# Kernel tuning notes

Hardware: AMD Instinct MI355X
Metric: run time of the kernel (lower is better)

The kernel has to match this reference:

```python
import jax, jax.numpy as jnp
import numpy as np
from jax.scipy.linalg import solve_triangular

N, K, D = 131072, 8, 32  # samples, clusters, dims


def setup_inputs() -> dict:
    key = jax.random.key(0)
    k1, k2, k3, k4 = jax.random.split(key, 4)
    return {
        "X": jax.random.normal(k1, (N, D), dtype=jnp.float32),
        "mu": jax.random.normal(k2, (K, D), dtype=jnp.float32),
        "L": jax.random.normal(k3, (K, D, D), dtype=jnp.float32),
        "weights": jax.random.normal(k4, (K,), dtype=jnp.float32),
        "it": 0,
    }


def _mixture_log_likelihoods(X, mu, L, weights):
    K_, D_ = mu.shape
    LOG2PI = float(np.log(2.0 * np.pi))
    # update_covariances: A_k = L_k L_k^T + I  (always SPD -> cholesky succeeds)
    A = jnp.einsum('kab,kcb->kac', L, L) + jnp.eye(D_, dtype=L.dtype)
    Lc = jnp.linalg.cholesky(A)            # [K,D,D] lower Cholesky factors
    invLc = jnp.linalg.inv(Lc)             # [K,D,D]
    # all cluster pairs (cartesian_prod order: i outer, j inner)
    ii, jj = [g.reshape(-1) for g in jnp.meshgrid(jnp.arange(K_), jnp.arange(K_), indexing='ij')]
    Si, Sj = Lc[ii], Lc[jj]                # NOTE: original uses the CHOLESKY FACTORS here
    invSi, invSj = invLc[ii], invLc[jj]
    mui, muj = mu[ii], mu[jj]
    # _gaussian_product: sigma = inv(inv(Si)+inv(Sj)); mu = sigma @ (inv(Si) mu_i + inv(Sj) mu_j)
    sigma = jnp.linalg.inv(invSi + invSj)                      # [P,D,D]
    rhs = jnp.einsum('pab,pb->pa', invSi, mui) + jnp.einsum('pab,pb->pa', invSj, muj)
    mu_p = jnp.einsum('pab,pb->pa', sigma, rhs)                # [P,D]
    # _product_z: log(1/sqrt(det(2*pi*(Si+Sj))) * exp(-0.5 dmu^T inv(Si+Sj) dmu))
    S = Si + Sj
    dmu = mui - muj
    quad = -0.5 * jnp.einsum('pa,pab,pb->p', dmu, jnp.linalg.inv(S), dmu)
    z = -0.5 * jnp.log(jnp.linalg.det(2.0 * np.pi * S)) + quad  # [P]
    # _unormalised_pdf: lower-triangular solve against sigma (only lower triangle used)
    diff = X[None, :, :] - mu_p[:, None, :]                    # [P,N,D]
    m = solve_triangular(sigma, jnp.swapaxes(diff, 1, 2), lower=True)  # [P,D,N]
    ll = -0.5 * (jnp.sum(m * m, axis=1) + D_ * LOG2PI
                 + jnp.log(jnp.linalg.det(sigma))[:, None])    # [P,N]
    logw = jax.nn.log_softmax(weights)                         # softmax weights, then log
    logprob = z[:, None] + ll + logw[ii][:, None] + logw[jj][:, None]  # [P,N]
    return jnp.log(jnp.sum(jnp.exp(logprob), axis=0))          # [N]


def reference(X, mu, L, weights, it):
    ll = _mixture_log_likelihoods(X, mu, L, weights)
    return jax.scipy.special.logsumexp(ll, axis=0)  # scalar
```

## Files before the change

kernel.cpp:

```cpp
#include <hip/hip_runtime.h>

#define D 32
#define K 8
#define NPAIR 36
#define PROWS 576

#define PMOFF 0
#define WOFF 4608
#define C2OFF 4864
#define CMAXOFF 4900
#define LCOFF 4928
#define PARTOFF 13120

typedef float v2f __attribute__((ext_vector_type(2)));

__host__ __device__ constexpr int gidx(int i, int j) {
    return i * 8 + j - i * (i + 1) / 2;
}
__host__ __device__ constexpr int proff(int r) {
    return 4 * (r / 4 + 1) * (2 * (r / 4) + (r % 4));
}

__global__ __launch_bounds__(64) void setup1_kernel(
    const float* __restrict__ mu, const float* __restrict__ L,
    float* __restrict__ ws)
{
    __shared__ float sA[D][D + 1];
    __shared__ float sLc[D][D + 1];
    __shared__ float sI[D][D + 1];
    const int k = blockIdx.x;
    const int tid = threadIdx.x;
    const int i = tid & 31;

    for (int e = tid; e < D * D; e += 64) sI[e >> 5][e & 31] = L[k * D * D + e];
    __syncthreads();

    for (int e = tid; e < D * D; e += 64) {
        const int a = e >> 5, c = e & 31;
        float s = (a == c) ? 1.0f : 0.0f;
        #pragma unroll
        for (int b = 0; b < D; ++b) s = fmaf(sI[a][b], sI[c][b], s);
        sA[a][c] = s;
    }
    __syncthreads();

    float lrow[D];
    #pragma unroll
    for (int j = 0; j < D; ++j) {
        if (i == j) {
            float s = sA[j][j];
            #pragma unroll
            for (int b = 0; b < j; ++b) s = fmaf(-lrow[b], lrow[b], s);
            const float d = sqrtf(s);
            lrow[j] = d;
            #pragma unroll
            for (int b = 0; b < j; ++b) sLc[j][b] = lrow[b];
            sLc[j][j] = d;
        }
        __syncthreads();
        if (i > j) {
            float s = sA[i][j];
            #pragma unroll
            for (int b = 0; b < j; ++b) s = fmaf(-lrow[b], sLc[j][b], s);
            lrow[j] = s / sLc[j][j];
        }
    }
    __syncthreads();

    for (int e = tid; e < D * D; e += 64) {
        const int r = e >> 5, c = e & 31;
        ws[LCOFF + k * D * D + e] = (c <= r) ? sLc[r][c] : 0.0f;
    }

    {
        const int j = i;
        #pragma unroll
        for (int ii = 0; ii < D; ++ii) {
            float s = (ii == j) ? 1.0f : 0.0f;
            #pragma unroll
            for (int b = 0; b < ii; ++b) s = fmaf(-sLc[ii][b], sI[b][j], s);
            const float cii = s / sLc[ii][ii];
            sI[ii][j] = cii;
            const int w4 = 4 * (ii / 4 + 1);
            if (j < w4) ws[PMOFF + k * PROWS + proff(ii) + j] = cii;
        }
    }
    __syncthreads();

    {
        float s = 0.0f;
        #pragma unroll
        for (int b = 0; b < D; ++b) s = fmaf(sI[i][b], mu[k * D + b], s);
        ws[WOFF + k * D + i] = s;
    }
}

#define SLC(kk, r, c) sLc2[(kk) * 1024 + (r) * 32 + (c)]

__global__ __launch_bounds__(64) void setup2_kernel(
    const float* __restrict__ mu, const float* __restrict__ weights,
    float* __restrict__ ws)
{
    __shared__ float sLc2[K * D * D];
    __shared__ float sLogw[K];
    __shared__ float sCp[NPAIR];
    __shared__ float sCmax;
    const int tid = threadIdx.x;

    {
        const float4* src = (const float4*)(ws + LCOFF);
        float4* dst = (float4*)sLc2;
        for (int e = tid; e < K * D * D / 4; e += 64) dst[e] = src[e];
    }
    if (tid == 0) {
        float m = -INFINITY;
        for (int t = 0; t < K; ++t) m = fmaxf(m, weights[t]);
        float s = 0.0f;
        for (int t = 0; t < K; ++t) s += expf(weights[t] - m);
        const float lse = m + logf(s);
        for (int t = 0; t < K; ++t) sLogw[t] = weights[t] - lse;
    }
    __syncthreads();

    if (tid < NPAIR) {
        int tt = tid, pi = 0;
        while (tt >= (K - pi)) { tt -= (K - pi); ++pi; }
        const int pj = pi + tt;
        const float LOG2PI = 1.8378770664093453f;
        float sumlogS = 0.0f, logdetsig = 0.0f;
        #pragma unroll
        for (int r = 0; r < D; ++r) {
            const float di = SLC(pi, r, r), dj = SLC(pj, r, r);
            sumlogS += logf(di + dj);
            logdetsig -= logf(1.0f / di + 1.0f / dj);
        }
        float v[D];
        float quad_acc = 0.0f;
        #pragma unroll
        for (int r = 0; r < D; ++r) {
            const float d0 = mu[pi * D + r] - mu[pj * D + r];
            float s = d0;
            #pragma unroll
            for (int b = 0; b < r; ++b)
                s = fmaf(-(SLC(pi, r, b) + SLC(pj, r, b)), v[b], s);
            v[r] = s / (SLC(pi, r, r) + SLC(pj, r, r));
            quad_acc = fmaf(d0, v[r], quad_acc);
        }
        const float quad = -0.5f * quad_acc;
        float c = quad - 0.5f * sumlogS - (float)D * LOG2PI - 0.5f * logdetsig
                  + sLogw[pi] + sLogw[pj];
        if (pi < pj) c += 0.6931471805599453f;
        sCp[tid] = c;
    }
    __syncthreads();
    if (tid == 0) {
        float m = -INFINITY;
        for (int t = 0; t < NPAIR; ++t) m = fmaxf(m, sCp[t]);
        sCmax = m;
        ws[CMAXOFF] = m;
    }
    __syncthreads();
    if (tid < NPAIR)
        ws[C2OFF + tid] = (sCp[tid] - sCmax) * 1.4426950408889634f;
}

__global__ __launch_bounds__(256, 1) void main_kernel(
    const float* __restrict__ X, const float* __restrict__ cst,
    float* __restrict__ partials, int nsamp)
{
    __shared__ __align__(16) float sM[K * PROWS];
    __shared__ __align__(16) float sW[K * D];
    __shared__ float sC2[NPAIR];
    __shared__ float sRed[4];
    const int tid = threadIdx.x;

    const int n0 = blockIdx.x * 512 + tid;
    const int n1 = n0 + 256;
    const int m0 = (n0 < nsamp) ? n0 : 0;
    const int m1 = (n1 < nsamp) ? n1 : 0;

    v2f xp[D];
    {
        const float4* Xv0 = (const float4*)(X + m0 * D);
        const float4* Xv1 = (const float4*)(X + m1 * D);
        #pragma unroll
        for (int q = 0; q < 8; ++q) {
            const float4 t0 = Xv0[q];
            const float4 t1 = Xv1[q];
            xp[4 * q + 0] = (v2f){t0.x, t1.x};
            xp[4 * q + 1] = (v2f){t0.y, t1.y};
            xp[4 * q + 2] = (v2f){t0.z, t1.z};
            xp[4 * q + 3] = (v2f){t0.w, t1.w};
        }
    }

    {
        const float4* src = (const float4*)cst;
        float4* dst = (float4*)sM;
        for (int e = tid; e < K * PROWS / 4; e += 256) dst[e] = src[e];
        const float4* srcw = (const float4*)(cst + WOFF);
        float4* dstw = (float4*)sW;
        if (tid < K * D / 4) dstw[tid] = srcw[tid];
        if (tid < NPAIR) sC2[tid] = cst[C2OFF + tid];
    }
    __syncthreads();

    v2f G2[NPAIR];
    #pragma unroll
    for (int t = 0; t < NPAIR; ++t) G2[t] = (v2f){0.0f, 0.0f};

    #pragma unroll
    for (int rh = 0; rh < 8; ++rh) {
        #pragma unroll
        for (int rr = 0; rr < 4; ++rr) {
            const int r = 4 * rh + rr;
            v2f y2[K];
            #pragma unroll
            for (int k = 0; k < K; ++k) {
                const float wv = sW[k * D + r];
                v2f a = (v2f){-wv, -wv};
                const float* Mr = sM + k * PROWS + proff(r);
                #pragma unroll
                for (int c4 = 0; c4 <= rh; ++c4) {
                    const float4 m4 = *(const float4*)(Mr + 4 * c4);
                    a = __builtin_elementwise_fma((v2f){m4.x, m4.x}, xp[4 * c4 + 0], a);
                    a = __builtin_elementwise_fma((v2f){m4.y, m4.y}, xp[4 * c4 + 1], a);
                    a = __builtin_elementwise_fma((v2f){m4.z, m4.z}, xp[4 * c4 + 2], a);
                    a = __builtin_elementwise_fma((v2f){m4.w, m4.w}, xp[4 * c4 + 3], a);
                }
                y2[k] = a;
            }
            #pragma unroll
            for (int pi = 0; pi < K; ++pi)
                #pragma unroll
                for (int pj = pi; pj < K; ++pj)
                    G2[gidx(pi, pj)] = __builtin_elementwise_fma(
                        y2[pi], y2[pj], G2[gidx(pi, pj)]);
        }
    }

    v2f acc2 = (v2f){0.0f, 0.0f};
    const float NH = -0.72134752044448170f;
    #pragma unroll
    for (int pi = 0; pi < K; ++pi)
        #pragma unroll
        for (int pj = pi; pj < K; ++pj) {
            const v2f q2 = __builtin_elementwise_fma(
                (v2f){2.0f, 2.0f}, G2[gidx(pi, pj)],
                G2[gidx(pi, pi)] + G2[gidx(pj, pj)]);
            const float c = sC2[gidx(pi, pj)];
            const v2f e2 = __builtin_elementwise_fma((v2f){NH, NH}, q2, (v2f){c, c});
            acc2.x += exp2f(e2.x);
            acc2.y += exp2f(e2.y);
        }
    float acc = ((n0 < nsamp) ? acc2.x : 0.0f) + ((n1 < nsamp) ? acc2.y : 0.0f);

    #pragma unroll
    for (int s = 1; s < 64; s <<= 1) acc += __shfl_xor(acc, s, 64);
    if ((tid & 63) == 0) sRed[tid >> 6] = acc;
    __syncthreads();
    if (tid == 0)
        partials[blockIdx.x] = sRed[0] + sRed[1] + sRed[2] + sRed[3];
}

__global__ __launch_bounds__(256) void finish_kernel(
    const float* __restrict__ partials, const float* __restrict__ ws,
    float* __restrict__ out, int nblk)
{
    __shared__ float sRed[4];
    const int tid = threadIdx.x;
    float acc = 0.0f;
    for (int e = tid; e < nblk; e += 256) acc += partials[e];
    #pragma unroll
    for (int s = 1; s < 64; s <<= 1) acc += __shfl_xor(acc, s, 64);
    if ((tid & 63) == 0) sRed[tid >> 6] = acc;
    __syncthreads();
    if (tid == 0) out[0] = ws[CMAXOFF] + logf(sRed[0] + sRed[1] + sRed[2] + sRed[3]);
}

extern "C" void kernel_launch(void* const* d_in, const int* in_sizes, int n_in,
                              void* d_out, int out_size, void* d_ws, size_t ws_size,
                              hipStream_t stream) {
    const float* X = (const float*)d_in[0];
    const float* mu = (const float*)d_in[1];
    const float* L = (const float*)d_in[2];
    const float* w = (const float*)d_in[3];
    float* wsf = (float*)d_ws;
    float* out = (float*)d_out;

    const int nsamp = in_sizes[0] / D;
    const int nblk = (nsamp + 511) / 512;

    setup1_kernel<<<K, 64, 0, stream>>>(mu, L, wsf);
    setup2_kernel<<<1, 64, 0, stream>>>(mu, w, wsf);
    main_kernel<<<nblk, 256, 0, stream>>>(X, wsf, wsf + PARTOFF, nsamp);
    finish_kernel<<<1, 256, 0, stream>>>(wsf + PARTOFF, wsf, out, nblk);
}
```

Before: 163.4 us.

## Split triangular-solve rows across two waves and merge Gram partials via LDS

Each block now holds 128 samples handled by two waves. The waves split the 8 row-groups of the triangular solve (even and odd row groups) and later merge their partial Gram accumulators through shared memory before the exp/sum step. The FMA layout also changes from pairing two samples per v2f to pairing adjacent dimensions, which needs an extra horizontal add. The aim is to raise parallelism and occupancy, since there are now 4x more blocks with two blocks allowed per CU. The cost is an LDS exchange of 36 float2 per lane, extra barriers, and an uneven load between the two waves, because the odd row groups have longer rows.

```diff
diff --git a/kernel.cpp b/kernel.cpp
--- a/kernel.cpp
+++ b/kernel.cpp
@@ -164,40 +164,43 @@
         ws[C2OFF + tid] = (sCp[tid] - sCmax) * 1.4426950408889634f;
 }
 
-__global__ __launch_bounds__(256, 1) void main_kernel(
+#define XCHG 4864
+
+__global__ __launch_bounds__(128, 2) void main_kernel(
     const float* __restrict__ X, const float* __restrict__ cst,
     float* __restrict__ partials, int nsamp)
 {
-    __shared__ __align__(16) float sM[K * PROWS];
+    __shared__ __align__(16) float sBig[XCHG];
     __shared__ __align__(16) float sW[K * D];
     __shared__ float sC2[NPAIR];
-    __shared__ float sRed[4];
     const int tid = threadIdx.x;
-
-    const int n0 = blockIdx.x * 512 + tid;
-    const int n1 = n0 + 256;
+    const int wv = tid >> 6;
+    const int lane = tid & 63;
+
+    const int n0 = blockIdx.x * 128 + lane;
+    const int n1 = n0 + 64;
     const int m0 = (n0 < nsamp) ? n0 : 0;
     const int m1 = (n1 < nsamp) ? n1 : 0;
 
-    v2f xp[D];
+    v2f xa[16], xb[16];
     {
         const float4* Xv0 = (const float4*)(X + m0 * D);
         const float4* Xv1 = (const float4*)(X + m1 * D);
         #pragma unroll
         for (int q = 0; q < 8; ++q) {
             const float4 t0 = Xv0[q];
+            xa[2 * q]     = (v2f){t0.x, t0.y};
+            xa[2 * q + 1] = (v2f){t0.z, t0.w};
             const float4 t1 = Xv1[q];
-            xp[4 * q + 0] = (v2f){t0.x, t1.x};
-            xp[4 * q + 1] = (v2f){t0.y, t1.y};
-            xp[4 * q + 2] = (v2f){t0.z, t1.z};
-            xp[4 * q + 3] = (v2f){t0.w, t1.w};
+            xb[2 * q]     = (v2f){t1.x, t1.y};
+            xb[2 * q + 1] = (v2f){t1.z, t1.w};
         }
     }
 
     {
         const float4* src = (const float4*)cst;
-        float4* dst = (float4*)sM;
-        for (int e = tid; e < K * PROWS / 4; e += 256) dst[e] = src[e];
+        float4* dst = (float4*)sBig;
+        for (int e = tid; e < K * PROWS / 4; e += 128) dst[e] = src[e];
         const float4* srcw = (const float4*)(cst + WOFF);
         float4* dstw = (float4*)sW;
         if (tid < K * D / 4) dstw[tid] = srcw[tid];
@@ -211,56 +214,83 @@
 
     #pragma unroll
     for (int rh = 0; rh < 8; ++rh) {
-        #pragma unroll
-        for (int rr = 0; rr < 4; ++rr) {
-            const int r = 4 * rh + rr;
-            v2f y2[K];
-            #pragma unroll
-            for (int k = 0; k < K; ++k) {
-                const float wv = sW[k * D + r];
-                v2f a = (v2f){-wv, -wv};
-                const float* Mr = sM + k * PROWS + proff(r);
+        if ((rh & 1) == wv) {
+            #pragma unroll
+            for (int rr = 0; rr < 4; ++rr) {
+                const int r = 4 * rh + rr;
+                v2f ya[K], yb[K];
                 #pragma unroll
-                for (int c4 = 0; c4 <= rh; ++c4) {
-                    const float4 m4 = *(const float4*)(Mr + 4 * c4);
-                    a = __builtin_elementwise_fma((v2f){m4.x, m4.x}, xp[4 * c4 + 0], a);
-                    a = __builtin_elementwise_fma((v2f){m4.y, m4.y}, xp[4 * c4 + 1], a);
-                    a = __builtin_elementwise_fma((v2f){m4.z, m4.z}, xp[4 * c4 + 2], a);
-                    a = __builtin_elementwise_fma((v2f){m4.w, m4.w}, xp[4 * c4 + 3], a);
+                for (int k = 0; k < K; ++k) {
+                    const float wvv = sW[k * D + r];
+                    v2f a0 = (v2f){-wvv, 0.0f};
+                    v2f a1 = (v2f){-wvv, 0.0f};
+                    const float* Mr = sBig + k * PROWS + proff(r);
+                    #pragma unroll
+                    for (int c4 = 0; c4 <= rh; ++c4) {
+                        const float4 m4 = *(const float4*)(Mr + 4 * c4);
+                        const v2f mlo = (v2f){m4.x, m4.y};
+                        const v2f mhi = (v2f){m4.z, m4.w};
+                        a0 = __builtin_elementwise_fma(mlo, xa[2 * c4],     a0);
+                        a1 = __builtin_elementwise_fma(mlo, xb[2 * c4],     a1);
+                        a0 = __builtin_elementwise_fma(mhi, xa[2 * c4 + 1], a0);
+                        a1 = __builtin_elementwise_fma(mhi, xb[2 * c4 + 1], a1);
+                    }
+                    ya[k] = a0;  yb[k] = a1;
                 }
-                y2[k] = a;
+                v2f y2[K];
+                #pragma unroll
+                for (int k = 0; k < K; ++k)
+                    y2[k] = (v2f){ya[k].x + ya[k].y, yb[k].x + yb[k].y};
+                #pragma unroll
+                for (int pi = 0; pi < K; ++pi)
+                    #pragma unroll
+                    for (int pj = pi; pj < K; ++pj)
+                        G2[gidx(pi, pj)] = __builtin_elementwise_fma(
+                            y2[pi], y2[pj], G2[gidx(pi, pj)]);
             }
-            #pragma unroll
-            for (int pi = 0; pi < K; ++pi)
-                #pragma unroll
-                for (int pj = pi; pj < K; ++pj)
-                    G2[gidx(pi, pj)] = __builtin_elementwise_fma(
-                        y2[pi], y2[pj], G2[gidx(pi, pj)]);
-        }
-    }
-
-    v2f acc2 = (v2f){0.0f, 0.0f};
-    const float NH = -0.72134752044448170f;
-    #pragma unroll
-    for (int pi = 0; pi < K; ++pi)
-        #pragma unroll
-        for (int pj = pi; pj < K; ++pj) {
-            const v2f q2 = __builtin_elementwise_fma(
-                (v2f){2.0f, 2.0f}, G2[gidx(pi, pj)],
-                G2[gidx(pi, pi)] + G2[gidx(pj, pj)]);
-            const float c = sC2[gidx(pi, pj)];
-            const v2f e2 = __builtin_elementwise_fma((v2f){NH, NH}, q2, (v2f){c, c});
-            acc2.x += exp2f(e2.x);
-            acc2.y += exp2f(e2.y);
-        }
-    float acc = ((n0 < nsamp) ? acc2.x : 0.0f) + ((n1 < nsamp) ? acc2.y : 0.0f);
-
-    #pragma unroll
-    for (int s = 1; s < 64; s <<= 1) acc += __shfl_xor(acc, s, 64);
-    if ((tid & 63) == 0) sRed[tid >> 6] = acc;
-    __syncthreads();
-    if (tid == 0)
-        partials[blockIdx.x] = sRed[0] + sRed[1] + sRed[2] + sRed[3];
+        }
+    }
+
+    __syncthreads();
+
+    if (wv == 1) {
+        float2* xch = (float2*)sBig;
+        #pragma unroll
+        for (int t = 0; t < NPAIR; ++t)
+            xch[t * 65 + lane] = make_float2(G2[t].x, G2[t].y);
+    }
+    __syncthreads();
+
+    if (wv == 0) {
+        const float2* xch = (const float2*)sBig;
+        #pragma unroll
+        for (int t = 0; t < NPAIR; ++t) {
+            const float2 g = xch[t * 65 + lane];
+            G2[t] += (v2f){g.x, g.y};
+        }
+
+        v2f acc2 = (v2f){0.0f, 0.0f};
+        const float NH = -0.72134752044448170f;
+        #pragma unroll
+        for (int pi = 0; pi < K; ++pi)
+            #pragma unroll
+            for (int pj = pi; pj < K; ++pj) {
+                const v2f q2 = __builtin_elementwise_fma(
+                    (v2f){2.0f, 2.0f}, G2[gidx(pi, pj)],
+                    G2[gidx(pi, pi)] + G2[gidx(pj, pj)]);
+                const float c = sC2[gidx(pi, pj)];
+                const v2f e2 = __builtin_elementwise_fma((v2f){NH, NH}, q2,
+                                                         (v2f){c, c});
+                acc2.x += exp2f(e2.x);
+                acc2.y += exp2f(e2.y);
+            }
+        float acc = ((n0 < nsamp) ? acc2.x : 0.0f)
+                  + ((n1 < nsamp) ? acc2.y : 0.0f);
+
+        #pragma unroll
+        for (int s = 1; s < 64; s <<= 1) acc += __shfl_xor(acc, s, 64);
+        if (lane == 0) partials[blockIdx.x] = acc;
+    }
 }
 
 __global__ __launch_bounds__(256) void finish_kernel(
@@ -289,10 +319,10 @@
     float* out = (float*)d_out;
 
     const int nsamp = in_sizes[0] / D;
-    const int nblk = (nsamp + 511) / 512;
+    const int nblk = (nsamp + 127) / 128;
 
     setup1_kernel<<<K, 64, 0, stream>>>(mu, L, wsf);
     setup2_kernel<<<1, 64, 0, stream>>>(mu, w, wsf);
-    main_kernel<<<nblk, 256, 0, stream>>>(X, wsf, wsf + PARTOFF, nsamp);
+    main_kernel<<<nblk, 128, 0, stream>>>(X, wsf, wsf + PARTOFF, nsamp);
     finish_kernel<<<1, 256, 0, stream>>>(wsf + PARTOFF, wsf, out, nblk);
 }
```

Result: faster. 146.1 us (-10.6%).
